# Optimization experiments

Hardware: AMD Instinct MI355X
Metric: run time of the kernel (lower is better)

Reference implementation:

```python
import jax, jax.numpy as jnp
import numpy as np
from jax import lax


def _maxpool_h(x):
    # MaxPool2d(kernel=(3,1), stride=(2,1), padding=(1,0)) on NCHW.
    # Torch pads with -inf for max pooling.
    return lax.reduce_window(
        x,
        -jnp.inf,
        lax.max,
        window_dimensions=(1, 1, 3, 1),
        window_strides=(1, 1, 2, 1),
        padding=((0, 0), (0, 0), (1, 1), (0, 0)),
    )


def setup_inputs() -> dict:
    key = jax.random.key(0)
    x = jax.random.normal(key, (32, 1, 8192, 256), dtype=jnp.float32)
    return {"x": x}


def reference(x) -> jnp.ndarray:
    out = _maxpool_h(x)  # [B, C, H', W]
    # Per-sample min-max normalization (vectorized over batch instead of the
    # original per-sample python loop).
    mx = jnp.max(out, axis=(1, 2, 3), keepdims=True)
    mn = jnp.min(out, axis=(1, 2, 3), keepdims=True)
    return (out - mn) / (mx - mn)
```

## Files before the change

### kernel.cpp

```cpp
#include <hip/hip_runtime.h>
#include <cfloat>

#define BATCH     32
#define H_IN      8192
#define H_OUT     4096
#define W         256
#define W4        64
#define CH        16
#define BLK_PER_B 64

typedef float f32x4 __attribute__((ext_vector_type(4)));

__device__ __forceinline__ float4 max3_f4(float4 a, float4 b, float4 c) {
    float4 m;
    m.x = fmaxf(a.x, fmaxf(b.x, c.x));
    m.y = fmaxf(a.y, fmaxf(b.y, c.y));
    m.z = fmaxf(a.z, fmaxf(b.z, c.z));
    m.w = fmaxf(a.w, fmaxf(b.w, c.w));
    return m;
}

__global__ __launch_bounds__(256) void pool_store_partial(
        const float* __restrict__ x, float* __restrict__ out,
        float* __restrict__ partial_min, float* __restrict__ partial_max) {
    const int batch = blockIdx.x >> 6;
    const int blk   = blockIdx.x & 63;
    const int tid   = threadIdx.x;
    const int w4    = tid & 63;
    const int rg    = tid >> 6;
    const int h0    = blk * (4 * CH) + rg * CH;

    const float4* xin = (const float4*)x + (size_t)batch * H_IN * W4 + w4;
    float4*       po  = (float4*)out + ((size_t)batch * H_OUT + h0) * W4 + w4;

    float lmin = FLT_MAX, lmax = -FLT_MAX;

    float4 prev;
    const int r0 = 2 * h0 - 1;
    if (r0 >= 0) prev = xin[(size_t)r0 * W4];
    else         prev = make_float4(-FLT_MAX, -FLT_MAX, -FLT_MAX, -FLT_MAX);

    #pragma unroll 4
    for (int i = 0; i < CH; ++i) {
        const int r = 2 * (h0 + i);
        float4 a = xin[(size_t)r * W4];
        float4 c = xin[(size_t)(r + 1) * W4];
        float4 m = max3_f4(prev, a, c);
        po[(size_t)i * W4] = m;
        prev = c;
        lmax = fmaxf(lmax, fmaxf(fmaxf(m.x, m.y), fmaxf(m.z, m.w)));
        lmin = fminf(lmin, fminf(fminf(m.x, m.y), fminf(m.z, m.w)));
    }

    #pragma unroll
    for (int off = 32; off > 0; off >>= 1) {
        lmax = fmaxf(lmax, __shfl_down(lmax, off, 64));
        lmin = fminf(lmin, __shfl_down(lmin, off, 64));
    }
    __shared__ float smax[4], smin[4];
    if ((tid & 63) == 0) { smax[rg] = lmax; smin[rg] = lmin; }
    __syncthreads();
    if (tid == 0) {
        float bmax = smax[0], bmin = smin[0];
        #pragma unroll
        for (int i = 1; i < 4; ++i) {
            bmax = fmaxf(bmax, smax[i]);
            bmin = fminf(bmin, smin[i]);
        }
        partial_max[blockIdx.x] = bmax;
        partial_min[blockIdx.x] = bmin;
    }
}

__global__ __launch_bounds__(256) void finish_normalize(
        float* __restrict__ out,
        const float* __restrict__ pmin, const float* __restrict__ pmax) {
    const int batch = blockIdx.x >> 6;
    const int blk   = blockIdx.x & 63;
    const int tid   = threadIdx.x;

    __shared__ float s_mn, s_inv;
    if (tid < 64) {
        float mn = pmin[batch * BLK_PER_B + tid];
        float mx = pmax[batch * BLK_PER_B + tid];
        #pragma unroll
        for (int off = 32; off > 0; off >>= 1) {
            mn = fminf(mn, __shfl_down(mn, off, 64));
            mx = fmaxf(mx, __shfl_down(mx, off, 64));
        }
        if (tid == 0) { s_mn = mn; s_inv = 1.0f / (mx - mn); }
    }
    __syncthreads();
    const float mn  = s_mn;
    const float inv = s_inv;

    f32x4* p = (f32x4*)out + (size_t)batch * (H_OUT * W4) + (size_t)blk * 4096;
    #pragma unroll 4
    for (int j = 0; j < 16; ++j) {
        const int idx = tid + j * 256;
        f32x4 v = p[idx];
        v.x = (v.x - mn) * inv;
        v.y = (v.y - mn) * inv;
        v.z = (v.z - mn) * inv;
        v.w = (v.w - mn) * inv;
        __builtin_nontemporal_store(v, p + idx);
    }
}

extern "C" void kernel_launch(void* const* d_in, const int* in_sizes, int n_in,
                              void* d_out, int out_size, void* d_ws, size_t ws_size,
                              hipStream_t stream) {
    const float* x   = (const float*)d_in[0];
    float*       out = (float*)d_out;
    float*       ws  = (float*)d_ws;

    float* pmin = ws;
    float* pmax = ws + 2048;

    pool_store_partial<<<BATCH * BLK_PER_B, 256, 0, stream>>>(x, out, pmin, pmax);
    finish_normalize<<<BATCH * BLK_PER_B, 256, 0, stream>>>(out, pmin, pmax);
}
```

Baseline: 427.1 us.

## Fuse pooling and normalization into a cooperative kernel with on-chip staging

Replaces the two-kernel pipeline, which wrote the pooled output and then read it back to normalize, with one cooperative kernel. Each of 512 blocks computes its pooled rows, keeps them in LDS (16 rows) and registers (48 rows), publishes per-block min/max, waits at a grid-wide sync, then normalizes and writes once. This removes a full read-modify-write pass over the 128 MB output. The cost is heavy LDS and register use, fewer and larger blocks, and a grid barrier; it falls back to the old path if the cooperative launch fails.

```diff
diff --git a/kernel.cpp b/kernel.cpp
--- a/kernel.cpp
+++ b/kernel.cpp
@@ -1,24 +1,132 @@
 #include <hip/hip_runtime.h>
+#include <hip/hip_cooperative_groups.h>
 #include <cfloat>
+
+namespace cg = cooperative_groups;
 
 #define BATCH     32
 #define H_IN      8192
 #define H_OUT     4096
-#define W         256
 #define W4        64
-#define CH        16
-#define BLK_PER_B 64
+#define BLK_PER_B 16
+#define NBLOCKS   (BATCH * BLK_PER_B)
+#define ROWS_BLK  (H_OUT / BLK_PER_B)
+#define CH        (ROWS_BLK / 4)
+#define NLDS      16
+#define NREG      (CH - NLDS)
 
 typedef float f32x4 __attribute__((ext_vector_type(4)));
 
-__device__ __forceinline__ float4 max3_f4(float4 a, float4 b, float4 c) {
-    float4 m;
+__device__ __forceinline__ f32x4 max3_f4(f32x4 a, f32x4 b, f32x4 c) {
+    f32x4 m;
     m.x = fmaxf(a.x, fmaxf(b.x, c.x));
     m.y = fmaxf(a.y, fmaxf(b.y, c.y));
     m.z = fmaxf(a.z, fmaxf(b.z, c.z));
     m.w = fmaxf(a.w, fmaxf(b.w, c.w));
     return m;
 }
+
+__global__ __launch_bounds__(256, 2) void fused_pool_norm(
+        const float* __restrict__ x, float* __restrict__ out,
+        float* __restrict__ pmin, float* __restrict__ pmax) {
+    const int bid   = blockIdx.x;
+    const int batch = bid >> 4;
+    const int blk   = bid & 15;
+    const int tid   = threadIdx.x;
+    const int w4    = tid & 63;
+    const int rg    = tid >> 6;
+    const int h0    = blk * ROWS_BLK + rg * CH;
+
+    __shared__ f32x4 lds4[NLDS * 256];
+    __shared__ float smax[4], smin[4];
+    __shared__ float s_mn, s_inv;
+
+    const f32x4* xin = (const f32x4*)x + (size_t)batch * H_IN * W4 + w4;
+
+    float lmin = FLT_MAX, lmax = -FLT_MAX;
+    f32x4 v[NREG];
+
+    f32x4 prev;
+    const int r0 = 2 * h0 - 1;
+    if (r0 >= 0) prev = xin[(size_t)r0 * W4];
+    else         prev = (f32x4){-FLT_MAX, -FLT_MAX, -FLT_MAX, -FLT_MAX};
+
+    #pragma unroll 4
+    for (int i = 0; i < NLDS; ++i) {
+        f32x4 a = xin[(size_t)(2 * (h0 + i)) * W4];
+        f32x4 c = xin[(size_t)(2 * (h0 + i) + 1) * W4];
+        f32x4 m = max3_f4(prev, a, c);
+        prev = c;
+        lmax = fmaxf(lmax, fmaxf(fmaxf(m.x, m.y), fmaxf(m.z, m.w)));
+        lmin = fminf(lmin, fminf(fminf(m.x, m.y), fminf(m.z, m.w)));
+        lds4[i * 256 + tid] = m;
+    }
+
+    #pragma unroll
+    for (int j = 0; j < NREG; ++j) {
+        const int i = NLDS + j;
+        f32x4 a = xin[(size_t)(2 * (h0 + i)) * W4];
+        f32x4 c = xin[(size_t)(2 * (h0 + i) + 1) * W4];
+        f32x4 m = max3_f4(prev, a, c);
+        prev = c;
+        lmax = fmaxf(lmax, fmaxf(fmaxf(m.x, m.y), fmaxf(m.z, m.w)));
+        lmin = fminf(lmin, fminf(fminf(m.x, m.y), fminf(m.z, m.w)));
+        v[j] = m;
+    }
+
+    #pragma unroll
+    for (int off = 32; off > 0; off >>= 1) {
+        lmax = fmaxf(lmax, __shfl_down(lmax, off, 64));
+        lmin = fminf(lmin, __shfl_down(lmin, off, 64));
+    }
+    if ((tid & 63) == 0) { smax[rg] = lmax; smin[rg] = lmin; }
+    __syncthreads();
+    if (tid == 0) {
+        float bmax = fmaxf(fmaxf(smax[0], smax[1]), fmaxf(smax[2], smax[3]));
+        float bmin = fminf(fminf(smin[0], smin[1]), fminf(smin[2], smin[3]));
+        __hip_atomic_store(&pmax[bid], bmax, __ATOMIC_RELEASE, __HIP_MEMORY_SCOPE_AGENT);
+        __hip_atomic_store(&pmin[bid], bmin, __ATOMIC_RELEASE, __HIP_MEMORY_SCOPE_AGENT);
+    }
+
+    cg::this_grid().sync();
+
+    if (tid < 64) {
+        float mn = (tid < BLK_PER_B)
+            ? __hip_atomic_load(&pmin[batch * BLK_PER_B + tid], __ATOMIC_ACQUIRE, __HIP_MEMORY_SCOPE_AGENT)
+            : FLT_MAX;
+        float mx = (tid < BLK_PER_B)
+            ? __hip_atomic_load(&pmax[batch * BLK_PER_B + tid], __ATOMIC_ACQUIRE, __HIP_MEMORY_SCOPE_AGENT)
+            : -FLT_MAX;
+        #pragma unroll
+        for (int off = 8; off > 0; off >>= 1) {
+            mn = fminf(mn, __shfl_down(mn, off, 64));
+            mx = fmaxf(mx, __shfl_down(mx, off, 64));
+        }
+        if (tid == 0) { s_mn = mn; s_inv = 1.0f / (mx - mn); }
+    }
+    __syncthreads();
+    const float mn  = s_mn;
+    const float inv = s_inv;
+
+    f32x4* po = (f32x4*)out + ((size_t)batch * H_OUT + h0) * W4 + w4;
+    #pragma unroll 4
+    for (int i = 0; i < NLDS; ++i) {
+        f32x4 m = lds4[i * 256 + tid];
+        f32x4 r = { (m.x - mn) * inv, (m.y - mn) * inv,
+                    (m.z - mn) * inv, (m.w - mn) * inv };
+        __builtin_nontemporal_store(r, po + (size_t)i * W4);
+    }
+    #pragma unroll
+    for (int j = 0; j < NREG; ++j) {
+        f32x4 m = v[j];
+        f32x4 r = { (m.x - mn) * inv, (m.y - mn) * inv,
+                    (m.z - mn) * inv, (m.w - mn) * inv };
+        __builtin_nontemporal_store(r, po + (size_t)(NLDS + j) * W4);
+    }
+}
+
+#define FB_BLK_PER_B 64
+#define FB_CH        16
 
 __global__ __launch_bounds__(256) void pool_store_partial(
         const float* __restrict__ x, float* __restrict__ out,
@@ -28,24 +136,24 @@
     const int tid   = threadIdx.x;
     const int w4    = tid & 63;
     const int rg    = tid >> 6;
-    const int h0    = blk * (4 * CH) + rg * CH;
-
-    const float4* xin = (const float4*)x + (size_t)batch * H_IN * W4 + w4;
-    float4*       po  = (float4*)out + ((size_t)batch * H_OUT + h0) * W4 + w4;
+    const int h0    = blk * (4 * FB_CH) + rg * FB_CH;
+
+    const f32x4* xin = (const f32x4*)x + (size_t)batch * H_IN * W4 + w4;
+    f32x4*       po  = (f32x4*)out + ((size_t)batch * H_OUT + h0) * W4 + w4;
 
     float lmin = FLT_MAX, lmax = -FLT_MAX;
 
-    float4 prev;
+    f32x4 prev;
     const int r0 = 2 * h0 - 1;
     if (r0 >= 0) prev = xin[(size_t)r0 * W4];
-    else         prev = make_float4(-FLT_MAX, -FLT_MAX, -FLT_MAX, -FLT_MAX);
-
-    #pragma unroll 4
-    for (int i = 0; i < CH; ++i) {
+    else         prev = (f32x4){-FLT_MAX, -FLT_MAX, -FLT_MAX, -FLT_MAX};
+
+    #pragma unroll 4
+    for (int i = 0; i < FB_CH; ++i) {
         const int r = 2 * (h0 + i);
-        float4 a = xin[(size_t)r * W4];
-        float4 c = xin[(size_t)(r + 1) * W4];
-        float4 m = max3_f4(prev, a, c);
+        f32x4 a = xin[(size_t)r * W4];
+        f32x4 c = xin[(size_t)(r + 1) * W4];
+        f32x4 m = max3_f4(prev, a, c);
         po[(size_t)i * W4] = m;
         prev = c;
         lmax = fmaxf(lmax, fmaxf(fmaxf(m.x, m.y), fmaxf(m.z, m.w)));
@@ -81,8 +189,8 @@
 
     __shared__ float s_mn, s_inv;
     if (tid < 64) {
-        float mn = pmin[batch * BLK_PER_B + tid];
-        float mx = pmax[batch * BLK_PER_B + tid];
+        float mn = pmin[batch * FB_BLK_PER_B + tid];
+        float mx = pmax[batch * FB_BLK_PER_B + tid];
         #pragma unroll
         for (int off = 32; off > 0; off >>= 1) {
             mn = fminf(mn, __shfl_down(mn, off, 64));
@@ -117,6 +225,12 @@
     float* pmin = ws;
     float* pmax = ws + 2048;
 
-    pool_store_partial<<<BATCH * BLK_PER_B, 256, 0, stream>>>(x, out, pmin, pmax);
-    finish_normalize<<<BATCH * BLK_PER_B, 256, 0, stream>>>(out, pmin, pmax);
-}
+    void* args[] = { (void*)&x, (void*)&out, (void*)&pmin, (void*)&pmax };
+    hipError_t err = hipLaunchCooperativeKernel(
+        (const void*)fused_pool_norm, dim3(NBLOCKS), dim3(256), args, 0, stream);
+
+    if (err != hipSuccess) {
+        pool_store_partial<<<BATCH * FB_BLK_PER_B, 256, 0, stream>>>(x, out, pmin, pmax);
+        finish_normalize<<<BATCH * FB_BLK_PER_B, 256, 0, stream>>>(out, pmin, pmax);
+    }
+}
```

Result: slower. 508.0 us (+18.9%).
